# Kernel optimization log

Measured on AMD Instinct MI355X. Metric: run time of the kernel, lower is better.

## Reference

```python
import jax, jax.numpy as jnp
import numpy as np

WINDOW_SIZE = 11
SIGMA = 1.5
C1 = 0.01 ** 2
C2 = 0.03 ** 2
ALPHA = 0.84


def _gaussian_window(window_size, sigma):
    x = np.arange(window_size, dtype=np.float32)
    g = np.exp(-((x - window_size // 2) ** 2) / (2.0 * sigma ** 2))
    g = g / g.sum()
    w2d = np.outer(g, g).astype(np.float32)  # [K, K]
    return jnp.asarray(w2d)


def _depthwise_conv(x, window):
    # x: [B, C, H, W]; window: [K, K] shared across channels (depthwise)
    C = x.shape[1]
    K = window.shape[0]
    kern = jnp.broadcast_to(window[None, None], (C, 1, K, K))  # [C, 1, K, K] OIHW
    pad = K // 2
    return jax.lax.conv_general_dilated(
        x, kern,
        window_strides=(1, 1),
        padding=((pad, pad), (pad, pad)),
        dimension_numbers=('NCHW', 'OIHW', 'NCHW'),
        feature_group_count=C,
    )


def _ssim(img1, img2):
    window = _gaussian_window(WINDOW_SIZE, SIGMA)
    mu1 = _depthwise_conv(img1, window)
    mu2 = _depthwise_conv(img2, window)
    mu1_sq = mu1 * mu1
    mu2_sq = mu2 * mu2
    mu1_mu2 = mu1 * mu2
    sigma1_sq = _depthwise_conv(img1 * img1, window) - mu1_sq
    sigma2_sq = _depthwise_conv(img2 * img2, window) - mu2_sq
    sigma12 = _depthwise_conv(img1 * img2, window) - mu1_mu2
    ssim_map = ((2 * mu1_mu2 + C1) * (2 * sigma12 + C2)) / (
        (mu1_sq + mu2_sq + C1) * (sigma1_sq + sigma2_sq + C2))
    return ssim_map.mean()


def setup_inputs() -> dict:
    key = jax.random.key(0)
    k1, k2 = jax.random.split(key)
    shape = (32, 3, 512, 512)
    pred = jax.random.uniform(k1, shape, dtype=jnp.float32)
    target = jax.random.uniform(k2, shape, dtype=jnp.float32)
    return {"pred": pred, "target": target}


def reference(pred, target):
    l1 = jnp.mean(jnp.abs(pred - target))
    s = _ssim(pred, target)
    return ALPHA * l1 + (1.0 - ALPHA) * (1.0 - s)
```

## Files before the change

### kernel.cpp

```cpp
#include <hip/hip_runtime.h>

#define SSIM_H 512
#define SSIM_W 512
#define PLANES 96
#define TILE 64
#define GRID_X (SSIM_W / TILE)
#define GRID_Y (SSIM_H / TILE)
#define TOTAL_BLOCKS (GRID_X * GRID_Y * PLANES)
#define N_TOTAL 25165824.0

typedef _Float16 half4v __attribute__((ext_vector_type(4)));
typedef _Float16 half8v __attribute__((ext_vector_type(8)));
typedef float float4v __attribute__((ext_vector_type(4)));

struct __align__(16) d2 { double x, y; };

__device__ __forceinline__ float gwf(int k) {
  const float d = (float)(k - 5);
  return __expf(-d * d / 4.5f) * 0.26601171702936207f;
}

__global__ __launch_bounds__(256, 4)
void ssim_l1_kernel(const float* __restrict__ pred,
                    const float* __restrict__ targ,
                    double* __restrict__ partials) {
  __shared__ _Float16 Hs[4][64][76];
  __shared__ float red[2][4];

  const int tid = (int)threadIdx.x;
  const int wv = tid >> 6;
  const int lane = tid & 63;
  const int q = lane >> 4;
  const int m = lane & 15;

  const int tr0 = (int)blockIdx.y * TILE;
  const int tc0 = (int)blockIdx.x * TILE;
  const size_t pbase = (size_t)blockIdx.z * (SSIM_H * SSIM_W);
  const float* __restrict__ xp = pred + pbase;
  const float* __restrict__ yp = targ + pbase;

  half8v wf;
#pragma unroll
  for (int j = 0; j < 8; ++j) {
    const int k = 8 * q + j - m;
    const float v = (k >= 0 && k <= 10) ? gwf(k) : 0.0f;
    wf[j] = (_Float16)v;
  }

  const int cw = tc0 + 16 * wv;
  const int cbase = cw - 5 + 8 * q;
  const bool cfast = (cbase >= 0) && (cbase + 7 < SSIM_W);

  float l1 = 0.0f;

#pragma unroll
  for (int rg = 0; rg < 5; ++rg) {
    const int grow = tr0 - 5 + rg * 16 + m;
    float xf[8], yf[8];
    if ((unsigned)grow < (unsigned)SSIM_H) {
      const float* __restrict__ xr = xp + (size_t)grow * SSIM_W;
      const float* __restrict__ yr = yp + (size_t)grow * SSIM_W;
      if (cfast) {
        float4 a0, a1, b0, b1;
        __builtin_memcpy(&a0, xr + cbase, 16);
        __builtin_memcpy(&a1, xr + cbase + 4, 16);
        __builtin_memcpy(&b0, yr + cbase, 16);
        __builtin_memcpy(&b1, yr + cbase + 4, 16);
        xf[0] = a0.x; xf[1] = a0.y; xf[2] = a0.z; xf[3] = a0.w;
        xf[4] = a1.x; xf[5] = a1.y; xf[6] = a1.z; xf[7] = a1.w;
        yf[0] = b0.x; yf[1] = b0.y; yf[2] = b0.z; yf[3] = b0.w;
        yf[4] = b1.x; yf[5] = b1.y; yf[6] = b1.z; yf[7] = b1.w;
      } else {
#pragma unroll
        for (int j = 0; j < 8; ++j) {
          const int c = cbase + j;
          const bool ok = (unsigned)c < (unsigned)SSIM_W;
          xf[j] = ok ? xr[c] : 0.0f;
          yf[j] = ok ? yr[c] : 0.0f;
        }
      }
    } else {
#pragma unroll
      for (int j = 0; j < 8; ++j) { xf[j] = 0.0f; yf[j] = 0.0f; }
    }

    const int hr = rg * 16 + m;
    if (hr >= 5 && hr < 69) {
#pragma unroll
      for (int j = 0; j < 8; ++j) {
        const int k = 8 * q + j;
        if (k >= 5 && k < 21) l1 += fabsf(xf[j] - yf[j]);
      }
    }

    half8v ax, ay, axxyy, axy;
#pragma unroll
    for (int j = 0; j < 8; ++j) {
      const float x = xf[j], y = yf[j];
      ax[j]    = (_Float16)x;
      ay[j]    = (_Float16)y;
      axxyy[j] = (_Float16)(x * x + y * y);
      axy[j]   = (_Float16)(x * y);
    }
    const float4v z = {0.0f, 0.0f, 0.0f, 0.0f};
    float4v c0 = __builtin_amdgcn_mfma_f32_16x16x32_f16(ax,    wf, z, 0, 0, 0);
    float4v c1 = __builtin_amdgcn_mfma_f32_16x16x32_f16(ay,    wf, z, 0, 0, 0);
    float4v c2 = __builtin_amdgcn_mfma_f32_16x16x32_f16(axxyy, wf, z, 0, 0, 0);
    float4v c3 = __builtin_amdgcn_mfma_f32_16x16x32_f16(axy,   wf, z, 0, 0, 0);

    if (rg != 4 || q != 3) {
      const int hcol = 16 * wv + m;
      const int hrow = rg * 16 + 4 * q;
      half4v h;
      h[0] = (_Float16)c0[0]; h[1] = (_Float16)c0[1];
      h[2] = (_Float16)c0[2]; h[3] = (_Float16)c0[3];
      *(half4v*)&Hs[0][hcol][hrow] = h;
      h[0] = (_Float16)c1[0]; h[1] = (_Float16)c1[1];
      h[2] = (_Float16)c1[2]; h[3] = (_Float16)c1[3];
      *(half4v*)&Hs[1][hcol][hrow] = h;
      h[0] = (_Float16)c2[0]; h[1] = (_Float16)c2[1];
      h[2] = (_Float16)c2[2]; h[3] = (_Float16)c2[3];
      *(half4v*)&Hs[2][hcol][hrow] = h;
      h[0] = (_Float16)c3[0]; h[1] = (_Float16)c3[1];
      h[2] = (_Float16)c3[2]; h[3] = (_Float16)c3[3];
      *(half4v*)&Hs[3][hcol][hrow] = h;
    }
  }

  asm volatile("s_waitcnt lgkmcnt(0)" ::: "memory");
  __builtin_amdgcn_sched_barrier(0);

  float ssim = 0.0f;
  {
    const int hcol = 16 * wv + m;
    half8v bfr[4][4];
#pragma unroll
    for (int rb = 0; rb < 4; ++rb) {
      const int hrow = 16 * rb + 8 * q;
      const int hrow_hi = (hrow + 4 <= 72) ? hrow + 4 : 72;
#pragma unroll
      for (int p = 0; p < 4; ++p) {
        half4v lo = *(const half4v*)&Hs[p][hcol][hrow];
        half4v hi = *(const half4v*)&Hs[p][hcol][hrow_hi];
        bfr[rb][p] = __builtin_shufflevector(lo, hi, 0, 1, 2, 3, 4, 5, 6, 7);
      }
    }
    const float C1v = 1.0e-4f, C2v = 9.0e-4f;
#pragma unroll
    for (int rb = 0; rb < 4; ++rb) {
      const float4v z = {0.0f, 0.0f, 0.0f, 0.0f};
      float4v acc[4];
#pragma unroll
      for (int p = 0; p < 4; ++p)
        acc[p] = __builtin_amdgcn_mfma_f32_16x16x32_f16(wf, bfr[rb][p], z,
                                                        0, 0, 0);
#pragma unroll
      for (int r = 0; r < 4; ++r) {
        const float mu1 = acc[0][r], mu2 = acc[1][r];
        const float exxyy = acc[2][r], exy = acc[3][r];
        const float m11 = mu1 * mu1, m22 = mu2 * mu2, m12 = mu1 * mu2;
        const float num = (2.0f * m12 + C1v) * (2.0f * (exy - m12) + C2v);
        const float den = (m11 + m22 + C1v) *
                          ((exxyy - m11 - m22) + C2v);
        ssim += num / den;
      }
    }
  }

  float v0 = l1, v1 = ssim;
#pragma unroll
  for (int off = 32; off > 0; off >>= 1) {
    v0 += __shfl_down(v0, off, 64);
    v1 += __shfl_down(v1, off, 64);
  }
  if (lane == 0) { red[0][wv] = v0; red[1][wv] = v1; }
  __syncthreads();
  if (tid == 0) {
    d2 s;
    s.x = (double)red[0][0] + (double)red[0][1] +
          (double)red[0][2] + (double)red[0][3];
    s.y = (double)red[1][0] + (double)red[1][1] +
          (double)red[1][2] + (double)red[1][3];
    const int bid = ((int)blockIdx.z * GRID_Y + (int)blockIdx.y) * GRID_X +
                    (int)blockIdx.x;
    *(d2*)(partials + 2 * bid) = s;
  }
}

__global__ __launch_bounds__(256)
void finalize_kernel(const double* __restrict__ partials,
                     float* __restrict__ out) {
  __shared__ double red[2][4];
  const int tid = (int)threadIdx.x;
  double L = 0.0, S = 0.0;
  for (int i = tid; i < TOTAL_BLOCKS; i += 256) {
    const d2 v = *(const d2*)(partials + 2 * i);
    L += v.x;
    S += v.y;
  }
#pragma unroll
  for (int off = 32; off > 0; off >>= 1) {
    L += __shfl_down(L, off, 64);
    S += __shfl_down(S, off, 64);
  }
  const int lane = tid & 63, wid = tid >> 6;
  if (lane == 0) { red[0][wid] = L; red[1][wid] = S; }
  __syncthreads();
  if (tid == 0) {
    const double Ls = red[0][0] + red[0][1] + red[0][2] + red[0][3];
    const double Ss = red[1][0] + red[1][1] + red[1][2] + red[1][3];
    const double invN = 1.0 / N_TOTAL;
    out[0] = (float)(0.84 * (Ls * invN) + 0.16 * (1.0 - Ss * invN));
  }
}

extern "C" void kernel_launch(void* const* d_in, const int* in_sizes, int n_in,
                              void* d_out, int out_size, void* d_ws, size_t ws_size,
                              hipStream_t stream) {
  const float* pred = (const float*)d_in[0];
  const float* targ = (const float*)d_in[1];
  float* out = (float*)d_out;
  double* partials = (double*)d_ws;

  dim3 grid(GRID_X, GRID_Y, PLANES);
  ssim_l1_kernel<<<grid, 256, 0, stream>>>(pred, targ, partials);
  finalize_kernel<<<1, 256, 0, stream>>>(partials, out);
}
```

Measured before the change: 252.2 us.

## Compute products in packed fp16, use 32-bit offsets, widen LDS reads

Computes x*x+y*y and x*y from the fp16-converted values with packed half vector math instead of in fp32 per element. Replaces 64-bit row pointer arithmetic with 32-bit shifted offsets on the fast load path. Merges the two 4-half LDS reads into single 8-half reads for the first three row blocks. Squaring in fp16 lowers the precision of the second-moment inputs, and the wider LDS reads may not be 16-byte aligned for every column.

```diff
diff --git a/kernel.cpp b/kernel.cpp
--- a/kernel.cpp
+++ b/kernel.cpp
@@ -58,19 +58,20 @@
     const int grow = tr0 - 5 + rg * 16 + m;
     float xf[8], yf[8];
     if ((unsigned)grow < (unsigned)SSIM_H) {
-      const float* __restrict__ xr = xp + (size_t)grow * SSIM_W;
-      const float* __restrict__ yr = yp + (size_t)grow * SSIM_W;
       if (cfast) {
+        const unsigned off = ((unsigned)grow << 9) + (unsigned)cbase;
         float4 a0, a1, b0, b1;
-        __builtin_memcpy(&a0, xr + cbase, 16);
-        __builtin_memcpy(&a1, xr + cbase + 4, 16);
-        __builtin_memcpy(&b0, yr + cbase, 16);
-        __builtin_memcpy(&b1, yr + cbase + 4, 16);
+        __builtin_memcpy(&a0, xp + off, 16);
+        __builtin_memcpy(&a1, xp + off + 4, 16);
+        __builtin_memcpy(&b0, yp + off, 16);
+        __builtin_memcpy(&b1, yp + off + 4, 16);
         xf[0] = a0.x; xf[1] = a0.y; xf[2] = a0.z; xf[3] = a0.w;
         xf[4] = a1.x; xf[5] = a1.y; xf[6] = a1.z; xf[7] = a1.w;
         yf[0] = b0.x; yf[1] = b0.y; yf[2] = b0.z; yf[3] = b0.w;
         yf[4] = b1.x; yf[5] = b1.y; yf[6] = b1.z; yf[7] = b1.w;
       } else {
+        const float* __restrict__ xr = xp + ((size_t)grow << 9);
+        const float* __restrict__ yr = yp + ((size_t)grow << 9);
 #pragma unroll
         for (int j = 0; j < 8; ++j) {
           const int c = cbase + j;
@@ -93,15 +94,15 @@
       }
     }
 
-    half8v ax, ay, axxyy, axy;
+    half8v ax, ay;
 #pragma unroll
     for (int j = 0; j < 8; ++j) {
-      const float x = xf[j], y = yf[j];
-      ax[j]    = (_Float16)x;
-      ay[j]    = (_Float16)y;
-      axxyy[j] = (_Float16)(x * x + y * y);
-      axy[j]   = (_Float16)(x * y);
-    }
+      ax[j] = (_Float16)xf[j];
+      ay[j] = (_Float16)yf[j];
+    }
+    half8v axxyy = ax * ax + ay * ay;
+    half8v axy = ax * ay;
+
     const float4v z = {0.0f, 0.0f, 0.0f, 0.0f};
     float4v c0 = __builtin_amdgcn_mfma_f32_16x16x32_f16(ax,    wf, z, 0, 0, 0);
     float4v c1 = __builtin_amdgcn_mfma_f32_16x16x32_f16(ay,    wf, z, 0, 0, 0);
@@ -135,14 +136,20 @@
     const int hcol = 16 * wv + m;
     half8v bfr[4][4];
 #pragma unroll
-    for (int rb = 0; rb < 4; ++rb) {
+    for (int rb = 0; rb < 3; ++rb) {
       const int hrow = 16 * rb + 8 * q;
+#pragma unroll
+      for (int p = 0; p < 4; ++p)
+        bfr[rb][p] = *(const half8v*)&Hs[p][hcol][hrow];
+    }
+    {
+      const int hrow = 48 + 8 * q;
       const int hrow_hi = (hrow + 4 <= 72) ? hrow + 4 : 72;
 #pragma unroll
       for (int p = 0; p < 4; ++p) {
         half4v lo = *(const half4v*)&Hs[p][hcol][hrow];
         half4v hi = *(const half4v*)&Hs[p][hcol][hrow_hi];
-        bfr[rb][p] = __builtin_shufflevector(lo, hi, 0, 1, 2, 3, 4, 5, 6, 7);
+        bfr[3][p] = __builtin_shufflevector(lo, hi, 0, 1, 2, 3, 4, 5, 6, 7);
       }
     }
     const float C1v = 1.0e-4f, C2v = 9.0e-4f;
```

Result: no change. 251.1 us (-0.4%).
